# Kernel optimization log

Hardware: AMD Instinct MI355X
Metric: run time of the kernel (lower is better)

## Reference

```python
import jax, jax.numpy as jnp
import numpy as np

D_MODEL = 512
NUM_HEADS = 8


def setup_inputs() -> dict:
    key = jax.random.key(0)
    ks = jax.random.split(key, 6)
    B, T, D = 4, 2048, D_MODEL
    x = jax.random.normal(ks[0], (B, T, D), dtype=jnp.float32)
    periods = jax.random.randint(ks[1], (B, NUM_HEADS), 0, 48)
    # nn.MultiheadAttention parameters: packed qkv in-projection + out-projection
    in_proj_w = jax.random.normal(ks[2], (3 * D, D), dtype=jnp.float32) * 0.02
    in_proj_b = jax.random.normal(ks[3], (3 * D,), dtype=jnp.float32) * 0.02
    out_w = jax.random.normal(ks[4], (D, D), dtype=jnp.float32) * 0.02
    out_b = jax.random.normal(ks[5], (D,), dtype=jnp.float32) * 0.02
    return {"x": x, "periods": periods, "in_proj_w": in_proj_w,
            "in_proj_b": in_proj_b, "out_w": out_w, "out_b": out_b}


def reference(x, periods, in_proj_w, in_proj_b, out_w, out_b):
    B, T, D = x.shape
    H = periods.shape[1]          # one head per period (num_heads == top_k)
    hd = D // H
    # packed qkv projection (matches torch in_proj_weight layout)
    qkv = x @ in_proj_w.T + in_proj_b            # (B,T,3D)
    q, k, v = jnp.split(qkv, 3, axis=-1)
    def to_heads(t):
        return t.reshape(B, T, H, hd).transpose(0, 2, 1, 3)  # (B,H,T,hd)
    q, k, v = to_heads(q), to_heads(k), to_heads(v)
    scores = jnp.einsum('bhqd,bhkd->bhqk', q, k) / jnp.sqrt(jnp.asarray(hd, x.dtype))
    # periodic causal mask: allow j<=i with (i-j) % P == 0
    i = jnp.arange(T)[:, None]
    j = jnp.arange(T)[None, :]
    p = jnp.maximum(periods, 1)[:, :, None, None]            # (B,H,1,1)
    allow = (j <= i) & (((i - j) % p) == 0)                  # (B,H,T,T)
    scores = jnp.where(allow, scores, -jnp.inf)              # diagonal always allowed -> no all-masked rows
    attn = jax.nn.softmax(scores, axis=-1)
    out = jnp.einsum('bhqk,bhkd->bhqd', attn, v)             # (B,H,T,hd)
    out = out.transpose(0, 2, 1, 3).reshape(B, T, D)
    return out @ out_w.T + out_b
```

## Files before the change

### kernel.cpp

```cpp
#include <hip/hip_runtime.h>
#include <math.h>

#define D_MODEL 512
#define NHEAD   8
#define HD      64
#define T_SEQ   2048
#define BATCH   4
#define M_ROWS  (BATCH * T_SEQ)

typedef __attribute__((ext_vector_type(8))) short        short8;
typedef __attribute__((ext_vector_type(4))) float        floatx4;
typedef __attribute__((ext_vector_type(4))) unsigned int uintx4;

__device__ __forceinline__ unsigned short f2bf(float f) {
    unsigned int u = __float_as_uint(f);
    unsigned int r = u + 0x7FFFu + ((u >> 16) & 1u);
    return (unsigned short)(r >> 16);
}

__device__ __forceinline__ float bf2f(unsigned short u) {
    return __uint_as_float((unsigned int)u << 16);
}

__device__ __forceinline__ float exp2_raw(float x) {
    float r;
    asm("v_exp_f32 %0, %1" : "=v"(r) : "v"(x));
    return r;
}

__device__ __forceinline__ int4 cvt8(float4 a, float4 b) {
    union { unsigned short u[8]; int4 v; } r;
    r.u[0] = f2bf(a.x); r.u[1] = f2bf(a.y); r.u[2] = f2bf(a.z); r.u[3] = f2bf(a.w);
    r.u[4] = f2bf(b.x); r.u[5] = f2bf(b.y); r.u[6] = f2bf(b.z); r.u[7] = f2bf(b.w);
    return r.v;
}

__device__ __forceinline__ void gload16(const void* g, void* l) {
    __builtin_amdgcn_global_load_lds(
        (const __attribute__((address_space(1))) void*)g,
        (__attribute__((address_space(3))) void*)l, 16, 0, 0);
}

__device__ __forceinline__ bool slot_decode(int t, int P, int& r, int& mt, int& Lr)
{
    const int q0 = T_SEQ / P, rem = T_SEQ % P;
    const int nt_hi = (q0 + 64) >> 6;
    const int nt_lo = (q0 + 63) >> 6;
    const int hi_total = rem * nt_hi;
    if (t < hi_total) {
        r = t / nt_hi; mt = t - r * nt_hi; Lr = q0 + 1;
    } else {
        t -= hi_total;
        if (t >= (P - rem) * nt_lo) return false;
        const int rr = t / nt_lo;
        r = rem + rr; mt = t - rr * nt_lo; Lr = q0;
    }
    return true;
}

#define XGROUPS  (M_ROWS * D_MODEL / 8)
#define W1GROUPS (3 * D_MODEL * D_MODEL / 8)
#define W2GROUPS (D_MODEL * D_MODEL / 8)
#define CVT_GROUPS (XGROUPS + W1GROUPS + W2GROUPS)
#define MAX_ITEMS 2560

__global__ __launch_bounds__(256) void cvt_inputs(
    const float* __restrict__ x, const float* __restrict__ w1,
    const float* __restrict__ w2, unsigned short* __restrict__ xo,
    unsigned short* __restrict__ w1o, unsigned short* __restrict__ w2o,
    const int* __restrict__ periods, int* __restrict__ items)
{
    {
        int i = blockIdx.x * 256 + threadIdx.x;
        const float* src; unsigned short* dst;
        if (i < XGROUPS)                  { src = x;  dst = xo;  }
        else if (i < XGROUPS + W1GROUPS)  { src = w1; dst = w1o; i -= XGROUPS; }
        else                              { src = w2; dst = w2o; i -= XGROUPS + W1GROUPS; }
        const float4* p = (const float4*)(src + (size_t)i * 8);
        float4 a = p[0], b = p[1];
        *(int4*)(dst + (size_t)i * 8) = cvt8(a, b);
    }
    if (blockIdx.x < 32) {
        const int bh = blockIdx.x;
        int P = periods[bh]; if (P < 1) P = 1;
        const int tid  = threadIdx.x;
        const int wave = tid >> 6, lane = tid & 63;
        const int t = 63 - (tid >> 2);
        const int c = 3 - (tid & 3);
        int r, mt, Lr;
        const bool valid = slot_decode(t, P, r, mt, Lr) && ((c << 3) <= mt);
        const unsigned long long mask = __ballot(valid);
        const int prefix = __popcll(mask & ((1ull << lane) - 1ull));
        __shared__ int wb[4];
        if (lane == 0) wb[wave] = __popcll(mask);
        if (tid < 80) items[bh * 80 + tid] = -1;
        __syncthreads();
        int base = 0;
        if (wave > 0) base += wb[0];
        if (wave > 1) base += wb[1];
        if (wave > 2) base += wb[2];
        if (valid) {
            const int rank = base + prefix;
            items[bh * 80 + ((rank + bh) % 80)] = (bh << 8) | (t << 2) | c;
        }
    }
}

__global__ __launch_bounds__(256) void qkv_gemm_mfma(
    const unsigned short* __restrict__ X,
    const unsigned short* __restrict__ W,
    const float* __restrict__ bias,
    unsigned short* __restrict__ qo, unsigned short* __restrict__ ko,
    unsigned short* __restrict__ vo)
{
    __shared__ unsigned short smem[128 * 128];
    unsigned short* const As = smem;
    unsigned short* const Bs = smem + 128 * 64;

    const int bid  = blockIdx.x;
    const int xcd  = bid & 7;
    const int chk_ = bid >> 3;
    const int row0 = (((chk_ / 12) << 3) + xcd) << 7;
    const int col0 = (chk_ % 12) << 7;

    const int tid  = threadIdx.x;
    const int wave = tid >> 6, lane = tid & 63;
    const int quad = lane >> 4, l15 = lane & 15;
    const int wm   = wave >> 1, wn = wave & 1;
    const int lr8  = lane >> 3;
    const int sc   = lane & 7;

    floatx4 acc[4][4] = {};

    for (int k0 = 0; k0 < D_MODEL; k0 += 64) {
#pragma unroll
        for (int i = 0; i < 4; ++i) {
            const int rb  = (wave << 5) + (i << 3);
            const int r   = rb + lr8;
            const int csw = sc ^ (r & 7);
            gload16(X + (size_t)(row0 + r) * D_MODEL + k0 + (csw << 3),
                    As + (rb << 6));
            gload16(W + (size_t)(col0 + r) * D_MODEL + k0 + (csw << 3),
                    Bs + (rb << 6));
        }
        __syncthreads();

#pragma unroll
        for (int ks = 0; ks < 2; ++ks) {
            short8 af[4], bfr[4];
            const int ch = (ks << 2) + quad;
#pragma unroll
            for (int mt = 0; mt < 4; ++mt) {
                const int row = (wm << 6) + (mt << 4) + l15;
                af[mt] = *(const short8*)(As + (row << 6) + ((ch ^ (row & 7)) << 3));
            }
#pragma unroll
            for (int nt = 0; nt < 4; ++nt) {
                const int col = (wn << 6) + (nt << 4) + l15;
                bfr[nt] = *(const short8*)(Bs + (col << 6) + ((ch ^ (col & 7)) << 3));
            }
#pragma unroll
            for (int mt = 0; mt < 4; ++mt)
#pragma unroll
                for (int nt = 0; nt < 4; ++nt)
                    acc[mt][nt] = __builtin_amdgcn_mfma_f32_16x16x32_bf16(
                        af[mt], bfr[nt], acc[mt][nt], 0, 0, 0);
        }
        __syncthreads();
    }

#pragma unroll
    for (int nt = 0; nt < 4; ++nt) {
        const int ncol = (wn << 6) + (nt << 4) + l15;
        const float bn = bias[col0 + ncol];
#pragma unroll
        for (int mt = 0; mt < 4; ++mt)
#pragma unroll
            for (int reg = 0; reg < 4; ++reg) {
                const int mrow = (wm << 6) + (mt << 4) + (quad << 2) + reg;
                smem[(mrow << 7) + ncol] = f2bf(acc[mt][nt][reg] + bn);
            }
    }
    __syncthreads();
    {
        const int c16  = lane & 15;
        const int rsub = lane >> 4;
        const int n0   = col0 + (c16 << 3);
        const int part = n0 >> 9;
        unsigned short* dst = (part == 0) ? qo : ((part == 1) ? ko : vo);
        const int head = (n0 & 511) >> 6, d0 = n0 & 63;
#pragma unroll
        for (int p = 0; p < 8; ++p) {
            const int ml = (wave << 5) + (p << 2) + rsub;
            const int m  = row0 + ml;
            const int b = m >> 11, t = m & 2047;
            int4 val = *(const int4*)(smem + (ml << 7) + (c16 << 3));
            *(int4*)(dst + ((((size_t)b << 3) + head) * T_SEQ + t) * HD + d0) = val;
        }
    }
}

#define SCALE2 0.18033688011112042f

__global__ __launch_bounds__(256) void attn_rc_mfma(
    const unsigned short* __restrict__ q, const unsigned short* __restrict__ k,
    const unsigned short* __restrict__ v, const int* __restrict__ periods,
    unsigned short* __restrict__ o,
    unsigned short* __restrict__ Opart, float* __restrict__ Lpart,
    const int* __restrict__ items)
{
    const int idx = items[blockIdx.x];
    if (idx < 0) return;

    __shared__ unsigned short Ks[2][64 * 64];
    __shared__ unsigned short Vt[2][64 * 64];

    const int bh     = idx >> 8;
    const int t_orig = (idx >> 2) & 63;
    const int c      = idx & 3;
    int P = periods[bh]; if (P < 1) P = 1;
    int r, mt, Lr;
    if (!slot_decode(t_orig, P, r, mt, Lr)) return;
    const int nch  = (mt >> 3) + 1;
    const int kt0  = c << 3;
    const int kend = (kt0 + 7 < mt) ? (kt0 + 7) : mt;
    const int m0   = mt << 6;

    const int tid  = threadIdx.x;
    const int wave = tid >> 6, lane = tid & 63;
    const int quad = lane >> 4, l15 = lane & 15;
    const int vkp  = tid & 31, vhg = tid >> 5;
    const int cpos = ((vkp >> 4) << 4) + (((vkp & 7) >> 1) << 2)
                   + (((vkp >> 3) & 1) << 1) + (vkp & 1);
    const int cgrp = cpos >> 2, clo = (cpos & 3) << 2;

    const unsigned short* hq = q + (size_t)bh * T_SEQ * HD;
    const unsigned short* hk = k + (size_t)bh * T_SEQ * HD;
    const unsigned short* hv = v + (size_t)bh * T_SEQ * HD;

    {
        const int km0 = kt0 << 6;
#pragma unroll
        for (int i = 0; i < 2; ++i) {
            const int rb  = (wave << 4) + (i << 3);
            const int rr  = rb + (lane >> 3);
            const int csw = ((lane & 7) ^ (rr & 7)) << 3;
            int mq = m0 + rr;  if (mq > Lr - 1) mq = Lr - 1;
            int mk = km0 + rr; if (mk > Lr - 1) mk = Lr - 1;
            gload16(hq + (size_t)(r + mq * P) * HD + csw, Ks[1] + (rb << 6));
            gload16(hk + (size_t)(r + mk * P) * HD + csw, Ks[0] + (rb << 6));
        }
        int mv0 = km0 + (vkp << 1);     if (mv0 > Lr - 1) mv0 = Lr - 1;
        int mv1 = km0 + (vkp << 1) + 1; if (mv1 > Lr - 1) mv1 = Lr - 1;
        int4 va = *(const int4*)(hv + (size_t)(r + mv0 * P) * HD + (vhg << 3));
        int4 vb = *(const int4*)(hv + (size_t)(r + mv1 * P) * HD + (vhg << 3));
        const unsigned short* pa = (const unsigned short*)&va;
        const unsigned short* pb = (const unsigned short*)&vb;
#pragma unroll
        for (int j = 0; j < 8; ++j) {
            const int hd_ = (vhg << 3) + j;
            const unsigned int pk =
                (unsigned int)pa[j] | ((unsigned int)pb[j] << 16);
            *(unsigned int*)((char*)Vt[0] + (hd_ << 7) +
                             ((cgrp ^ (hd_ & 7)) << 4) + clo) = pk;
        }
    }
    __syncthreads();
    short8 qf[2];
#pragma unroll
    for (int ks = 0; ks < 2; ++ks) {
        const int row = (wave << 4) + l15;
        qf[ks] = *(const short8*)(Ks[1] + (row << 6) +
                                  ((((ks << 2) + quad) ^ (row & 7)) << 3));
    }
    __syncthreads();

    floatx4 Oa[4] = {};
    float Lacc = 0.f;
    const int qrel = (wave << 4) + l15;

    for (int kt = kt0; kt <= kend; ++kt) {
        const int buf = (kt - kt0) & 1;
        const bool havenext = kt < kend;

        int4 va, vb;
        if (havenext) {
            const int km0 = (kt + 1) << 6;
#pragma unroll
            for (int i = 0; i < 2; ++i) {
                const int rb  = (wave << 4) + (i << 3);
                const int rr  = rb + (lane >> 3);
                int mk = km0 + rr; if (mk > Lr - 1) mk = Lr - 1;
                gload16(hk + (size_t)(r + mk * P) * HD +
                            (((lane & 7) ^ (rr & 7)) << 3),
                        Ks[buf ^ 1] + (rb << 6));
            }
            int mv0 = km0 + (vkp << 1);     if (mv0 > Lr - 1) mv0 = Lr - 1;
            int mv1 = km0 + (vkp << 1) + 1; if (mv1 > Lr - 1) mv1 = Lr - 1;
            va = *(const int4*)(hv + (size_t)(r + mv0 * P) * HD + (vhg << 3));
            vb = *(const int4*)(hv + (size_t)(r + mv1 * P) * HD + (vhg << 3));
        }

        floatx4 sacc[4] = {};
        __builtin_amdgcn_s_setprio(1);
#pragma unroll
        for (int nt = 0; nt < 4; ++nt) {
            const int row = (nt << 4) + l15;
#pragma unroll
            for (int ks = 0; ks < 2; ++ks) {
                short8 kf = *(const short8*)(Ks[buf] + (row << 6) +
                                             ((((ks << 2) + quad) ^ (row & 7)) << 3));
                sacc[nt] = __builtin_amdgcn_mfma_f32_16x16x32_bf16(
                    kf, qf[ks], sacc[nt], 0, 0, 0);
            }
        }
        __builtin_amdgcn_s_setprio(0);

        const bool diag = (kt == mt);
        unsigned int wv[8];
        float rs = 0.f;
#pragma unroll
        for (int nt = 0; nt < 4; ++nt) {
            unsigned short bq[4];
#pragma unroll
            for (int reg = 0; reg < 4; ++reg) {
                const int krel = (nt << 4) + (quad << 2) + reg;
                float sv = fmaf(sacc[nt][reg], SCALE2, -8.f);
                if (diag && krel > qrel) sv = -1e30f;
                bq[reg] = f2bf(exp2_raw(sv));
                rs += bf2f(bq[reg]);
            }
            wv[(nt << 1)]     = (unsigned int)bq[0] | ((unsigned int)bq[1] << 16);
            wv[(nt << 1) | 1] = (unsigned int)bq[2] | ((unsigned int)bq[3] << 16);
        }
        Lacc += rs;
        uintx4 wA = {wv[0], wv[1], wv[2], wv[3]};
        uintx4 wB = {wv[4], wv[5], wv[6], wv[7]};
        const short8 pa0 = __builtin_bit_cast(short8, wA);
        const short8 pa1 = __builtin_bit_cast(short8, wB);

        __builtin_amdgcn_s_setprio(1);
#pragma unroll
        for (int nt = 0; nt < 4; ++nt) {
            const int row = (nt << 4) + l15;
#pragma unroll
            for (int ks = 0; ks < 2; ++ks) {
                short8 vf = *(const short8*)(Vt[buf] + (row << 6) +
                                             ((((ks << 2) + quad) ^ (row & 7)) << 3));
                Oa[nt] = __builtin_amdgcn_mfma_f32_16x16x32_bf16(
                    ks ? pa1 : pa0, vf, Oa[nt], 0, 0, 0);
            }
        }
        __builtin_amdgcn_s_setprio(0);

        if (havenext) {
            const unsigned short* pa = (const unsigned short*)&va;
            const unsigned short* pb = (const unsigned short*)&vb;
#pragma unroll
            for (int j = 0; j < 8; ++j) {
                const int hd_ = (vhg << 3) + j;
                const unsigned int pk =
                    (unsigned int)pa[j] | ((unsigned int)pb[j] << 16);
                *(unsigned int*)((char*)Vt[buf ^ 1] + (hd_ << 7) +
                                 ((cgrp ^ (hd_ & 7)) << 4) + clo) = pk;
            }
        }
        __syncthreads();
    }

    Lacc += __shfl_xor(Lacc, 16);
    Lacc += __shfl_xor(Lacc, 32);
    float l_i[4];
#pragma unroll
    for (int reg = 0; reg < 4; ++reg)
        l_i[reg] = __shfl(Lacc, (lane & 48) | (quad << 2) | reg);

    if (nch == 1) {
#pragma unroll
        for (int reg = 0; reg < 4; ++reg) {
            const float invl = 1.f / l_i[reg];
            const int row = (wave << 4) + (quad << 2) + reg;
#pragma unroll
            for (int nt = 0; nt < 4; ++nt)
                Ks[0][(row << 6) + (nt << 4) + l15] = f2bf(Oa[nt][reg] * invl);
        }
        const int lrow = lane >> 2;
        const int chk  = (lane & 3) << 1;
        const int ml   = (wave << 4) + lrow;
        const int m    = m0 + ml;
        if (m < Lr) {
            const size_t base = ((size_t)bh * T_SEQ + (r + m * P)) * HD;
            int4 w0 = *(const int4*)(Ks[0] + (ml << 6) + (chk << 3));
            int4 w1 = *(const int4*)(Ks[0] + (ml << 6) + ((chk + 1) << 3));
            *(int4*)(o + base + (chk << 3))       = w0;
            *(int4*)(o + base + ((chk + 1) << 3)) = w1;
        }
    } else {
        const size_t slot = ((size_t)((bh << 6) + t_orig) << 2) + c;
#pragma unroll
        for (int reg = 0; reg < 4; ++reg) {
            const int row = (wave << 4) + (quad << 2) + reg;
#pragma unroll
            for (int nt = 0; nt < 4; ++nt)
                Ks[0][(row << 6) + (nt << 4) + l15] = f2bf(Oa[nt][reg]);
            if (l15 == 0)
                Lpart[slot * 64 + row] = l_i[reg];
        }
        const int lrow = lane >> 2;
        const int chk  = (lane & 3) << 1;
        const int ml   = (wave << 4) + lrow;
        unsigned short* dst = Opart + slot * 4096 + (ml << 6);
        *(int4*)(dst + (chk << 3))       = *(const int4*)(Ks[0] + (ml << 6) + (chk << 3));
        *(int4*)(dst + ((chk + 1) << 3)) = *(const int4*)(Ks[0] + (ml << 6) + ((chk + 1) << 3));
    }
}

__global__ __launch_bounds__(256) void reduce_rc(
    const int* __restrict__ periods,
    const unsigned short* __restrict__ Opart, const float* __restrict__ Lpart,
    unsigned short* __restrict__ o)
{
    const int bh = blockIdx.y;
    int P = periods[bh]; if (P < 1) P = 1;
    const int t = blockIdx.x;
    int r, mt, Lr;
    if (!slot_decode(t, P, r, mt, Lr)) return;
    const int nch = (mt >> 3) + 1;
    if (nch < 2) return;

    const int tid = threadIdx.x;
    const int row = tid >> 2;
    const int cg  = (tid & 3) << 4;
    const int m   = (mt << 6) + row;
    if (m >= Lr) return;

    const size_t slot0 = (size_t)((bh << 6) + t) << 2;

    float lsum = 0.f;
    for (int cc = 0; cc < nch; ++cc)
        lsum += Lpart[(slot0 + cc) * 64 + row];
    const float inv = 1.f / lsum;

    float ov[16] = {};
    for (int cc = 0; cc < nch; ++cc) {
        const unsigned short* p = Opart + (slot0 + cc) * 4096 + (row << 6) + cg;
#pragma unroll
        for (int j = 0; j < 16; ++j) ov[j] += bf2f(p[j]);
    }
    unsigned short outv[16];
#pragma unroll
    for (int j = 0; j < 16; ++j) outv[j] = f2bf(ov[j] * inv);

    unsigned short* dst = o + ((size_t)bh * T_SEQ + (r + m * P)) * HD + cg;
    *(int4*)dst       = *(const int4*)&outv[0];
    *(int4*)(dst + 8) = *(const int4*)&outv[8];
}

__global__ __launch_bounds__(256) void out_gemm_mfma(
    const unsigned short* __restrict__ A,
    const unsigned short* __restrict__ W,
    const float* __restrict__ bias,
    float* __restrict__ out)
{
    __shared__ unsigned short As[64 * 64];
    __shared__ unsigned short Bs[128 * 64];

    const int tid  = threadIdx.x;
    const int wave = tid >> 6, lane = tid & 63;
    const int quad = lane >> 4, l15 = lane & 15;
    const int wm   = wave >> 1, wn = wave & 1;
    const int row0 = blockIdx.x * 64;
    const int col0 = blockIdx.y * 128;
    const int lr8  = lane >> 3;
    const int sc   = lane & 7;

    floatx4 acc[2][4] = {};

    for (int k0 = 0; k0 < D_MODEL; k0 += 64) {
        const int h = k0 >> 6;
#pragma unroll
        for (int i = 0; i < 4; ++i) {
            const int rb  = (wave << 5) + (i << 3);
            const int r   = rb + lr8;
            const int csw = sc ^ (r & 7);
            gload16(W + (size_t)(col0 + r) * D_MODEL + k0 + (csw << 3),
                    Bs + (rb << 6));
        }
#pragma unroll
        for (int i = 0; i < 2; ++i) {
            const int rb  = (wave << 4) + (i << 3);
            const int r   = rb + lr8;
            const int csw = sc ^ (r & 7);
            const int rg = row0 + r;
            const int b = rg >> 11, t = rg & 2047;
            gload16(A + ((((size_t)b << 3) + h) * T_SEQ + t) * HD + (csw << 3),
                    As + (rb << 6));
        }
        __syncthreads();

#pragma unroll
        for (int ks = 0; ks < 2; ++ks) {
            short8 af[2], bfr[4];
            const int ch = (ks << 2) + quad;
#pragma unroll
            for (int mt = 0; mt < 2; ++mt) {
                const int row = (wm << 5) + (mt << 4) + l15;
                af[mt] = *(const short8*)(As + (row << 6) + ((ch ^ (row & 7)) << 3));
            }
#pragma unroll
            for (int nt = 0; nt < 4; ++nt) {
                const int col = (wn << 6) + (nt << 4) + l15;
                bfr[nt] = *(const short8*)(Bs + (col << 6) + ((ch ^ (col & 7)) << 3));
            }
#pragma unroll
            for (int mt = 0; mt < 2; ++mt)
#pragma unroll
                for (int nt = 0; nt < 4; ++nt)
                    acc[mt][nt] = __builtin_amdgcn_mfma_f32_16x16x32_bf16(
                        af[mt], bfr[nt], acc[mt][nt], 0, 0, 0);
        }
        __syncthreads();
    }

#pragma unroll
    for (int nt = 0; nt < 4; ++nt) {
        const int n = col0 + (wn << 6) + (nt << 4) + l15;
        const float bn = bias[n];
#pragma unroll
        for (int mt = 0; mt < 2; ++mt) {
#pragma unroll
            for (int reg = 0; reg < 4; ++reg) {
                const int m = row0 + (wm << 5) + (mt << 4) + (quad << 2) + reg;
                out[(size_t)m * D_MODEL + n] = acc[mt][nt][reg] + bn;
            }
        }
    }
}

extern "C" void kernel_launch(void* const* d_in, const int* in_sizes, int n_in,
                              void* d_out, int out_size, void* d_ws, size_t ws_size,
                              hipStream_t stream)
{
    const float* x        = (const float*)d_in[0];
    const int*   periods  = (const int*)  d_in[1];
    const float* in_w     = (const float*)d_in[2];
    const float* in_b     = (const float*)d_in[3];
    const float* out_w    = (const float*)d_in[4];
    const float* out_b    = (const float*)d_in[5];
    float*       out      = (float*)d_out;

    const size_t TENS = (size_t)BATCH * NHEAD * T_SEQ * HD;
    unsigned short* qb    = (unsigned short*)d_ws;
    unsigned short* kb    = qb + TENS;
    unsigned short* vb    = kb + TENS;
    unsigned short* aob   = vb + TENS;
    unsigned short* Opart = aob + TENS;
    float*          Lpart = (float*)(Opart + (size_t)8192 * 4096);
    unsigned short* Xb    = (unsigned short*)(Lpart + (size_t)8192 * 64);
    unsigned short* W1b   = Xb + (size_t)M_ROWS * D_MODEL;
    unsigned short* W2b   = W1b + (size_t)3 * D_MODEL * D_MODEL;
    int*            items = (int*)(W2b + (size_t)D_MODEL * D_MODEL);

    cvt_inputs<<<CVT_GROUPS / 256, 256, 0, stream>>>(x, in_w, out_w,
                                                     Xb, W1b, W2b,
                                                     periods, items);

    qkv_gemm_mfma<<<(M_ROWS / 128) * ((3 * D_MODEL) / 128), 256, 0, stream>>>(
        Xb, W1b, in_b, qb, kb, vb);

    attn_rc_mfma<<<MAX_ITEMS, 256, 0, stream>>>(qb, kb, vb, periods, aob,
                                                Opart, Lpart, items);
    reduce_rc<<<dim3(64, BATCH * NHEAD), 256, 0, stream>>>(
        periods, Opart, Lpart, aob);

    dim3 g3(M_ROWS / 64, D_MODEL / 128);
    out_gemm_mfma<<<g3, 256, 0, stream>>>(aob, W2b, out_b, out);
}
```

Measured before the change: 135.8 us.

## Drop split-K chunking in periodic attention and remove the reduce kernel

Each attention work item now handles a whole residue-class query tile over all of its key tiles, so the split into chunks of up to 8 key tiles goes away. This removes the partial O/L buffers, the separate reduce_rc launch and its global traffic, and normalises the output directly. The cost is less parallelism and worse load balance: long residue classes (small P) become long single blocks that can dominate the tail, and fewer items are launched.

```diff
diff --git a/kernel.cpp b/kernel.cpp
--- a/kernel.cpp
+++ b/kernel.cpp
@@ -62,7 +62,7 @@
 #define W1GROUPS (3 * D_MODEL * D_MODEL / 8)
 #define W2GROUPS (D_MODEL * D_MODEL / 8)
 #define CVT_GROUPS (XGROUPS + W1GROUPS + W2GROUPS)
-#define MAX_ITEMS 2560
+#define MAX_ITEMS 2048
 
 __global__ __launch_bounds__(256) void cvt_inputs(
     const float* __restrict__ x, const float* __restrict__ w1,
@@ -83,25 +83,18 @@
     if (blockIdx.x < 32) {
         const int bh = blockIdx.x;
         int P = periods[bh]; if (P < 1) P = 1;
-        const int tid  = threadIdx.x;
-        const int wave = tid >> 6, lane = tid & 63;
-        const int t = 63 - (tid >> 2);
-        const int c = 3 - (tid & 3);
-        int r, mt, Lr;
-        const bool valid = slot_decode(t, P, r, mt, Lr) && ((c << 3) <= mt);
-        const unsigned long long mask = __ballot(valid);
-        const int prefix = __popcll(mask & ((1ull << lane) - 1ull));
-        __shared__ int wb[4];
-        if (lane == 0) wb[wave] = __popcll(mask);
-        if (tid < 80) items[bh * 80 + tid] = -1;
+        const int tid = threadIdx.x;
+        if (tid < 64) items[bh * 64 + tid] = -1;
         __syncthreads();
-        int base = 0;
-        if (wave > 0) base += wb[0];
-        if (wave > 1) base += wb[1];
-        if (wave > 2) base += wb[2];
-        if (valid) {
-            const int rank = base + prefix;
-            items[bh * 80 + ((rank + bh) % 80)] = (bh << 8) | (t << 2) | c;
+        if (tid < 64) {
+            const int lane = tid;
+            const int t = 63 - lane;
+            int r, mt, Lr;
+            const bool valid = slot_decode(t, P, r, mt, Lr);
+            const unsigned long long mask = __ballot(valid);
+            const int rank = __popcll(mask & ((1ull << lane) - 1ull));
+            if (valid)
+                items[bh * 64 + ((rank + bh) & 63)] = (bh << 8) | (t << 2);
         }
     }
 }
@@ -205,9 +198,7 @@
 __global__ __launch_bounds__(256) void attn_rc_mfma(
     const unsigned short* __restrict__ q, const unsigned short* __restrict__ k,
     const unsigned short* __restrict__ v, const int* __restrict__ periods,
-    unsigned short* __restrict__ o,
-    unsigned short* __restrict__ Opart, float* __restrict__ Lpart,
-    const int* __restrict__ items)
+    unsigned short* __restrict__ o, const int* __restrict__ items)
 {
     const int idx = items[blockIdx.x];
     if (idx < 0) return;
@@ -217,13 +208,10 @@
 
     const int bh     = idx >> 8;
     const int t_orig = (idx >> 2) & 63;
-    const int c      = idx & 3;
     int P = periods[bh]; if (P < 1) P = 1;
     int r, mt, Lr;
     if (!slot_decode(t_orig, P, r, mt, Lr)) return;
-    const int nch  = (mt >> 3) + 1;
-    const int kt0  = c << 3;
-    const int kend = (kt0 + 7 < mt) ? (kt0 + 7) : mt;
+    const int kend = mt;
     const int m0   = mt << 6;
 
     const int tid  = threadIdx.x;
@@ -239,19 +227,18 @@
     const unsigned short* hv = v + (size_t)bh * T_SEQ * HD;
 
     {
-        const int km0 = kt0 << 6;
 #pragma unroll
         for (int i = 0; i < 2; ++i) {
             const int rb  = (wave << 4) + (i << 3);
             const int rr  = rb + (lane >> 3);
             const int csw = ((lane & 7) ^ (rr & 7)) << 3;
-            int mq = m0 + rr;  if (mq > Lr - 1) mq = Lr - 1;
-            int mk = km0 + rr; if (mk > Lr - 1) mk = Lr - 1;
+            int mq = m0 + rr; if (mq > Lr - 1) mq = Lr - 1;
+            int mk = rr;      if (mk > Lr - 1) mk = Lr - 1;
             gload16(hq + (size_t)(r + mq * P) * HD + csw, Ks[1] + (rb << 6));
             gload16(hk + (size_t)(r + mk * P) * HD + csw, Ks[0] + (rb << 6));
         }
-        int mv0 = km0 + (vkp << 1);     if (mv0 > Lr - 1) mv0 = Lr - 1;
-        int mv1 = km0 + (vkp << 1) + 1; if (mv1 > Lr - 1) mv1 = Lr - 1;
+        int mv0 = (vkp << 1);     if (mv0 > Lr - 1) mv0 = Lr - 1;
+        int mv1 = (vkp << 1) + 1; if (mv1 > Lr - 1) mv1 = Lr - 1;
         int4 va = *(const int4*)(hv + (size_t)(r + mv0 * P) * HD + (vhg << 3));
         int4 vb = *(const int4*)(hv + (size_t)(r + mv1 * P) * HD + (vhg << 3));
         const unsigned short* pa = (const unsigned short*)&va;
@@ -279,8 +266,8 @@
     float Lacc = 0.f;
     const int qrel = (wave << 4) + l15;
 
-    for (int kt = kt0; kt <= kend; ++kt) {
-        const int buf = (kt - kt0) & 1;
+    for (int kt = 0; kt <= kend; ++kt) {
+        const int buf = kt & 1;
         const bool havenext = kt < kend;
 
         int4 va, vb;
@@ -375,85 +362,25 @@
     for (int reg = 0; reg < 4; ++reg)
         l_i[reg] = __shfl(Lacc, (lane & 48) | (quad << 2) | reg);
 
-    if (nch == 1) {
-#pragma unroll
-        for (int reg = 0; reg < 4; ++reg) {
-            const float invl = 1.f / l_i[reg];
-            const int row = (wave << 4) + (quad << 2) + reg;
-#pragma unroll
-            for (int nt = 0; nt < 4; ++nt)
-                Ks[0][(row << 6) + (nt << 4) + l15] = f2bf(Oa[nt][reg] * invl);
-        }
-        const int lrow = lane >> 2;
-        const int chk  = (lane & 3) << 1;
-        const int ml   = (wave << 4) + lrow;
-        const int m    = m0 + ml;
-        if (m < Lr) {
-            const size_t base = ((size_t)bh * T_SEQ + (r + m * P)) * HD;
-            int4 w0 = *(const int4*)(Ks[0] + (ml << 6) + (chk << 3));
-            int4 w1 = *(const int4*)(Ks[0] + (ml << 6) + ((chk + 1) << 3));
-            *(int4*)(o + base + (chk << 3))       = w0;
-            *(int4*)(o + base + ((chk + 1) << 3)) = w1;
-        }
-    } else {
-        const size_t slot = ((size_t)((bh << 6) + t_orig) << 2) + c;
-#pragma unroll
-        for (int reg = 0; reg < 4; ++reg) {
-            const int row = (wave << 4) + (quad << 2) + reg;
-#pragma unroll
-            for (int nt = 0; nt < 4; ++nt)
-                Ks[0][(row << 6) + (nt << 4) + l15] = f2bf(Oa[nt][reg]);
-            if (l15 == 0)
-                Lpart[slot * 64 + row] = l_i[reg];
-        }
-        const int lrow = lane >> 2;
-        const int chk  = (lane & 3) << 1;
-        const int ml   = (wave << 4) + lrow;
-        unsigned short* dst = Opart + slot * 4096 + (ml << 6);
-        *(int4*)(dst + (chk << 3))       = *(const int4*)(Ks[0] + (ml << 6) + (chk << 3));
-        *(int4*)(dst + ((chk + 1) << 3)) = *(const int4*)(Ks[0] + (ml << 6) + ((chk + 1) << 3));
-    }
-}
-
-__global__ __launch_bounds__(256) void reduce_rc(
-    const int* __restrict__ periods,
-    const unsigned short* __restrict__ Opart, const float* __restrict__ Lpart,
-    unsigned short* __restrict__ o)
-{
-    const int bh = blockIdx.y;
-    int P = periods[bh]; if (P < 1) P = 1;
-    const int t = blockIdx.x;
-    int r, mt, Lr;
-    if (!slot_decode(t, P, r, mt, Lr)) return;
-    const int nch = (mt >> 3) + 1;
-    if (nch < 2) return;
-
-    const int tid = threadIdx.x;
-    const int row = tid >> 2;
-    const int cg  = (tid & 3) << 4;
-    const int m   = (mt << 6) + row;
-    if (m >= Lr) return;
-
-    const size_t slot0 = (size_t)((bh << 6) + t) << 2;
-
-    float lsum = 0.f;
-    for (int cc = 0; cc < nch; ++cc)
-        lsum += Lpart[(slot0 + cc) * 64 + row];
-    const float inv = 1.f / lsum;
-
-    float ov[16] = {};
-    for (int cc = 0; cc < nch; ++cc) {
-        const unsigned short* p = Opart + (slot0 + cc) * 4096 + (row << 6) + cg;
-#pragma unroll
-        for (int j = 0; j < 16; ++j) ov[j] += bf2f(p[j]);
-    }
-    unsigned short outv[16];
-#pragma unroll
-    for (int j = 0; j < 16; ++j) outv[j] = f2bf(ov[j] * inv);
-
-    unsigned short* dst = o + ((size_t)bh * T_SEQ + (r + m * P)) * HD + cg;
-    *(int4*)dst       = *(const int4*)&outv[0];
-    *(int4*)(dst + 8) = *(const int4*)&outv[8];
+#pragma unroll
+    for (int reg = 0; reg < 4; ++reg) {
+        const float invl = 1.f / l_i[reg];
+        const int row = (wave << 4) + (quad << 2) + reg;
+#pragma unroll
+        for (int nt = 0; nt < 4; ++nt)
+            Ks[0][(row << 6) + (nt << 4) + l15] = f2bf(Oa[nt][reg] * invl);
+    }
+    const int lrow = lane >> 2;
+    const int chk  = (lane & 3) << 1;
+    const int ml   = (wave << 4) + lrow;
+    const int m    = m0 + ml;
+    if (m < Lr) {
+        const size_t base = ((size_t)bh * T_SEQ + (r + m * P)) * HD;
+        int4 w0 = *(const int4*)(Ks[0] + (ml << 6) + (chk << 3));
+        int4 w1 = *(const int4*)(Ks[0] + (ml << 6) + ((chk + 1) << 3));
+        *(int4*)(o + base + (chk << 3))       = w0;
+        *(int4*)(o + base + ((chk + 1) << 3)) = w1;
+    }
 }
 
 __global__ __launch_bounds__(256) void out_gemm_mfma(
@@ -554,9 +481,7 @@
     unsigned short* kb    = qb + TENS;
     unsigned short* vb    = kb + TENS;
     unsigned short* aob   = vb + TENS;
-    unsigned short* Opart = aob + TENS;
-    float*          Lpart = (float*)(Opart + (size_t)8192 * 4096);
-    unsigned short* Xb    = (unsigned short*)(Lpart + (size_t)8192 * 64);
+    unsigned short* Xb    = aob + TENS;
     unsigned short* W1b   = Xb + (size_t)M_ROWS * D_MODEL;
     unsigned short* W2b   = W1b + (size_t)3 * D_MODEL * D_MODEL;
     int*            items = (int*)(W2b + (size_t)D_MODEL * D_MODEL);
@@ -569,9 +494,7 @@
         Xb, W1b, in_b, qb, kb, vb);
 
     attn_rc_mfma<<<MAX_ITEMS, 256, 0, stream>>>(qb, kb, vb, periods, aob,
-                                                Opart, Lpart, items);
-    reduce_rc<<<dim3(64, BATCH * NHEAD), 256, 0, stream>>>(
-        periods, Opart, Lpart, aob);
+                                                items);
 
     dim3 g3(M_ROWS / 64, D_MODEL / 128);
     out_gemm_mfma<<<g3, 256, 0, stream>>>(aob, W2b, out_b, out);
```

Result: slower. 162.6 us (+19.8%).
